# Optimization experiments

Measured on AMD Instinct MI355X. Metric: run time of the kernel, lower is better.

Reference implementation:

```python
import jax, jax.numpy as jnp
import numpy as np

N_NODES = 100000
N_EDGES = 1600000
D = 128


def setup_inputs() -> dict:
    key = jax.random.key(0)
    k1, k2, k3, k4 = jax.random.split(key, 4)
    ego_embeddings = jax.random.normal(k1, (N_NODES, D), dtype=jnp.float32)
    edge_index = jax.random.randint(k2, (2, N_EDGES), 0, N_NODES, dtype=jnp.int64)
    edge_weight = jax.random.uniform(k3, (N_EDGES,), dtype=jnp.float32)
    W = jax.random.normal(k4, (D, D), dtype=jnp.float32) * (1.0 / np.sqrt(D))
    b = jnp.zeros((D,), dtype=jnp.float32)
    return {"ego_embeddings": ego_embeddings, "edge_index": edge_index,
            "edge_weight": edge_weight, "W": W, "b": b}


def reference(ego_embeddings, edge_index, edge_weight, W, b):
    # SpMM: side[i] = sum_j A[i,j] * ego[j], A given as COO (dst=row, src=col)
    src = edge_index[1]
    dst = edge_index[0]
    messages = ego_embeddings[src] * edge_weight[:, None]  # [E, D]
    side_embeddings = jax.ops.segment_sum(messages, dst, num_segments=N_NODES)
    # gcn aggregator: LeakyReLU(Linear(ego + side)); dropout p=0.0 -> identity
    h = (ego_embeddings + side_embeddings) @ W.T + b
    return jax.nn.leaky_relu(h, negative_slope=0.01)
```

## Files before the change

kernel.cpp:

```cpp
#include <hip/hip_runtime.h>

#define N_NODES 100000
#define N_EDGES 1600000
#define DIM 128
#define CAP 48

#define NBIN 1563
#define BINW 64
#define BCAP 1280
#define EPB  8192
#define NBBLK ((N_EDGES + EPB - 1) / EPB)

#define WB_OFF   0
#define GCUR_OFF 32768
#define STG_OFF  65536
#define EGOB_OFF (STG_OFF + (size_t)NBIN * BCAP * 8)
#define WS_BF16  (EGOB_OFF + (size_t)N_NODES * DIM * 2)

#define DEG_OFF  65536
#define EPK_OFF  465536

using short8  = __attribute__((ext_vector_type(8))) short;
using floatx4 = __attribute__((ext_vector_type(4))) float;

static __device__ __forceinline__ unsigned short f2bf(float f) {
    unsigned u = __float_as_uint(f);
    u += 0x7FFF + ((u >> 16) & 1);
    return (unsigned short)(u >> 16);
}
static __device__ __forceinline__ float bf_lo(unsigned u) {
    return __uint_as_float(u << 16);
}
static __device__ __forceinline__ float bf_hi(unsigned u) {
    return __uint_as_float(u & 0xFFFF0000u);
}

#define EGO_BLKS 6250
#define TAIL_BLKS 64
__global__ __launch_bounds__(256) void convert_all(
        const float4* __restrict__ e4, uint4* __restrict__ o4,
        const float* __restrict__ W, unsigned short* __restrict__ Wb,
        int* __restrict__ gcur) {
    const int b = blockIdx.x;
    const int tid = threadIdx.x;
    if (b < EGO_BLKS) {
        int i = b * 256 + tid;
        float4 a = e4[2 * i];
        float4 c = e4[2 * i + 1];
        uint4 o;
        o.x = (unsigned)f2bf(a.x) | ((unsigned)f2bf(a.y) << 16);
        o.y = (unsigned)f2bf(a.z) | ((unsigned)f2bf(a.w) << 16);
        o.z = (unsigned)f2bf(c.x) | ((unsigned)f2bf(c.y) << 16);
        o.w = (unsigned)f2bf(c.z) | ((unsigned)f2bf(c.w) << 16);
        o4[i] = o;
    } else {
        int j = (b - EGO_BLKS) * 256 + tid;
        if (j < DIM * DIM) Wb[j] = f2bf(W[j]);
        if (j < NBIN) gcur[j] = 0;
    }
}

__global__ __launch_bounds__(256) void convert_w(const float* __restrict__ W,
                                                 unsigned short* __restrict__ Wb) {
    int i = blockIdx.x * 256 + threadIdx.x;
    if (i < DIM * DIM) Wb[i] = f2bf(W[i]);
}

__global__ __launch_bounds__(256) void bin2scan(
        const int* __restrict__ eidx,
        const float* __restrict__ ew,
        int* __restrict__ gcur,
        uint2* __restrict__ stg) {
    __shared__ int lh[NBIN];
    __shared__ int gb[NBIN];
    const int tid = threadIdx.x;
    const int b0 = blockIdx.x * EPB;

    for (int i = tid; i < NBIN; i += 256) lh[i] = 0;
    __syncthreads();

    for (int k = 0; k < EPB / 256; ++k) {
        int e = b0 + k * 256 + tid;
        if (e < N_EDGES) atomicAdd(&lh[eidx[e] >> 6], 1);
    }
    __syncthreads();

    for (int i = tid; i < NBIN; i += 256) {
        int c = lh[i];
        gb[i] = c ? atomicAdd(&gcur[i], c) : 0;
        lh[i] = 0;
    }
    __syncthreads();

    for (int k = 0; k < EPB / 256; ++k) {
        int e = b0 + k * 256 + tid;
        if (e < N_EDGES) {
            int d = eidx[e];
            int s = eidx[N_EDGES + e];
            float w = ew[e];
            unsigned rec = ((unsigned)s << 15) | (unsigned)(w * 32767.0f + 0.5f);
            int bin = d >> 6;
            int pos = gb[bin] + atomicAdd(&lh[bin], 1);
            if (pos < BCAP)
                stg[(size_t)bin * BCAP + pos] = make_uint2(rec, (unsigned)d);
        }
    }
}

#define LSTR 136
__global__ __launch_bounds__(256, 5) void bin_gather_gemm(
        const unsigned* __restrict__ eg2,
        const uint2* __restrict__ stg,
        const int* __restrict__ gcur,
        const unsigned short* __restrict__ Wb,
        const float* __restrict__ bias,
        float* __restrict__ out) {
    __shared__ __align__(16) unsigned short s_x[BINW * LSTR];
    __shared__ unsigned s_epk[BINW * CAP];
    __shared__ int s_lc[BINW];

    const int tid  = threadIdx.x;
    const int wave = tid >> 6;
    const int lane = tid & 63;
    const int bin  = blockIdx.x;
    const int R    = bin * BINW;
    const float inv15 = 1.0f / 32767.0f;
    const uint2* eg8 = (const uint2*)eg2;

    if (tid < BINW) s_lc[tid] = 0;
    __syncthreads();

    int cnt = gcur[bin];
    if (cnt > BCAP) cnt = BCAP;
    const uint2* bstg = stg + (size_t)bin * BCAP;
    for (int r = tid; r < cnt; r += 256) {
        uint2 rc = bstg[r];
        int d6 = (int)(rc.y & (BINW - 1));
        int rk = atomicAdd(&s_lc[d6], 1);
        if (rk < CAP) s_epk[d6 * CAP + rk] = rc.x;
    }
    __syncthreads();

    {
        const int half = lane >> 5;
        const int hl   = lane & 31;
        const int plane = (lane < CAP) ? lane : (CAP - 1);

        int lA = wave * 16;
        unsigned pvA = s_epk[lA * CAP + plane];
        unsigned pvB = s_epk[(lA + 1) * CAP + plane];
        int dgA = s_lc[lA];
        int dgB = s_lc[lA + 1];

        for (int i = 0; i < 8; ++i) {
            const int myNode = R + wave * 16 + 2 * i + half;
            const bool valid = myNode < N_NODES;

            unsigned pvAc = pvA, pvBc = pvB;
            int dgAc = dgA < CAP ? dgA : CAP;
            int dgBc = dgB < CAP ? dgB : CAP;
            const int dgme = half ? dgBc : dgAc;
            const int dgw  = dgAc > dgBc ? dgAc : dgBc;

            if (i < 7) {
                int mA = wave * 16 + 2 * (i + 1);
                pvA = s_epk[mA * CAP + plane];
                pvB = s_epk[(mA + 1) * CAP + plane];
                dgA = s_lc[mA];
                dgB = s_lc[mA + 1];
            }

            uint2 idv = make_uint2(0u, 0u);
            if (valid) idv = eg8[(size_t)myNode * 32 + hl];

            float acc[4][4];
#pragma unroll
            for (int k = 0; k < 4; ++k)
#pragma unroll
                for (int c = 0; c < 4; ++c) acc[k][c] = 0.f;
            acc[0][0] = bf_lo(idv.x);  acc[0][1] = bf_hi(idv.x);
            acc[0][2] = bf_lo(idv.y);  acc[0][3] = bf_hi(idv.y);

            for (int e = 0; e < dgw; e += 8) {
                unsigned p[8];
                uint2 g[8];
#pragma unroll
                for (int k = 0; k < 8; ++k) {
                    unsigned pa = __shfl(pvAc, e + k);
                    unsigned pb = __shfl(pvBc, e + k);
                    unsigned ps = half ? pb : pa;
                    p[k] = ((e + k) < dgme) ? ps : 0u;
                }
#pragma unroll
                for (int k = 0; k < 8; ++k)
                    g[k] = eg8[(size_t)(p[k] >> 15) * 32 + hl];
#pragma unroll
                for (int k = 0; k < 8; ++k) {
                    float wv = (float)(p[k] & 0x7FFF) * inv15;
                    acc[k & 3][0] = fmaf(wv, bf_lo(g[k].x), acc[k & 3][0]);
                    acc[k & 3][1] = fmaf(wv, bf_hi(g[k].x), acc[k & 3][1]);
                    acc[k & 3][2] = fmaf(wv, bf_lo(g[k].y), acc[k & 3][2]);
                    acc[k & 3][3] = fmaf(wv, bf_hi(g[k].y), acc[k & 3][3]);
                }
            }

            float s0 = (acc[0][0] + acc[1][0]) + (acc[2][0] + acc[3][0]);
            float s1 = (acc[0][1] + acc[1][1]) + (acc[2][1] + acc[3][1]);
            float s2 = (acc[0][2] + acc[1][2]) + (acc[2][2] + acc[3][2]);
            float s3 = (acc[0][3] + acc[1][3]) + (acc[2][3] + acc[3][3]);

            unsigned lo = (unsigned)f2bf(s0) | ((unsigned)f2bf(s1) << 16);
            unsigned hi = (unsigned)f2bf(s2) | ((unsigned)f2bf(s3) << 16);
            int myRow = wave * 16 + 2 * i + half;
            *(uint2*)&s_x[myRow * LSTR + hl * 4] = make_uint2(lo, hi);
        }
    }

    const int m0 = wave * 16;
    const int ml = lane & 15;
    const int q  = lane >> 4;

    floatx4 acc[8];
#pragma unroll
    for (int nt = 0; nt < 8; ++nt) acc[nt] = (floatx4){0.f, 0.f, 0.f, 0.f};

#pragma unroll
    for (int kc = 0; kc < 4; ++kc) {
        short8 a = *(const short8*)&s_x[(m0 + ml) * LSTR + kc * 32 + q * 8];
#pragma unroll
        for (int nt = 0; nt < 8; ++nt) {
            short8 b = *(const short8*)&Wb[(size_t)(nt * 16 + ml) * DIM + kc * 32 + q * 8];
            acc[nt] = __builtin_amdgcn_mfma_f32_16x16x32_bf16(a, b, acc[nt], 0, 0, 0);
        }
    }

#pragma unroll
    for (int nt = 0; nt < 8; ++nt) {
        int col = nt * 16 + ml;
        float bv = bias[col];
#pragma unroll
        for (int r = 0; r < 4; ++r) {
            int row = R + m0 + q * 4 + r;
            if (row < N_NODES) {
                float v = acc[nt][r] + bv;
                v = v > 0.f ? v : 0.01f * v;
                out[(size_t)row * DIM + col] = v;
            }
        }
    }
}

__global__ __launch_bounds__(256) void csr_scatter(
        const int* __restrict__ eidx,
        const float* __restrict__ ew,
        int* __restrict__ deg,
        unsigned* __restrict__ epk) {
    int e = blockIdx.x * 256 + threadIdx.x;
    if (e >= N_EDGES) return;
    int dst = eidx[e];
    int src = eidx[N_EDGES + e];
    float w = ew[e];
    int r = atomicAdd(&deg[dst], 1);
    if (r < CAP) {
        unsigned q = (unsigned)(w * 32767.0f + 0.5f);
        epk[(size_t)dst * CAP + r] = ((unsigned)src << 15) | q;
    }
}

__global__ __launch_bounds__(256) void gather_gemm_f32(
        const float* __restrict__ egof,
        const unsigned* __restrict__ epk,
        const int* __restrict__ deg,
        const unsigned short* __restrict__ Wb,
        const float* __restrict__ bias,
        float* __restrict__ out) {
    __shared__ __align__(16) unsigned short s_x[64 * LSTR];

    const int tid  = threadIdx.x;
    const int wave = tid >> 6;
    const int lane = tid & 63;
    const int R    = blockIdx.x * 64;
    const float inv15 = 1.0f / 32767.0f;

    for (int i = 0; i < 16; ++i) {
        int node = R + wave * 16 + i;
        float ax = 0.f, ay = 0.f, bx = 0.f, by = 0.f;
        float cx = 0.f, cy = 0.f, dx2 = 0.f, dy2 = 0.f;
        if (node < N_NODES) {
            size_t cidx = (size_t)node * 64 + lane;
            float2 vv = ((const float2*)egof)[cidx];
            ax = vv.x; ay = vv.y;
            int dg = deg[node];
            if (dg > CAP) dg = CAP;
            size_t base = (size_t)node * CAP;
            unsigned pv = epk[base + (lane < CAP ? lane : CAP - 1)];
            int e = 0;
            for (; e + 3 < dg; e += 4) {
                unsigned p0 = __shfl(pv, e + 0);
                unsigned p1 = __shfl(pv, e + 1);
                unsigned p2 = __shfl(pv, e + 2);
                unsigned p3 = __shfl(pv, e + 3);
                float2 v0 = ((const float2*)egof)[(size_t)(p0 >> 15) * 64 + lane];
                float2 v1 = ((const float2*)egof)[(size_t)(p1 >> 15) * 64 + lane];
                float2 v2 = ((const float2*)egof)[(size_t)(p2 >> 15) * 64 + lane];
                float2 v3 = ((const float2*)egof)[(size_t)(p3 >> 15) * 64 + lane];
                float w0 = (float)(p0 & 0x7FFF) * inv15;
                float w1 = (float)(p1 & 0x7FFF) * inv15;
                float w2 = (float)(p2 & 0x7FFF) * inv15;
                float w3 = (float)(p3 & 0x7FFF) * inv15;
                ax = fmaf(w0, v0.x, ax);  ay = fmaf(w0, v0.y, ay);
                bx = fmaf(w1, v1.x, bx);  by = fmaf(w1, v1.y, by);
                cx = fmaf(w2, v2.x, cx);  cy = fmaf(w2, v2.y, cy);
                dx2 = fmaf(w3, v3.x, dx2); dy2 = fmaf(w3, v3.y, dy2);
            }
            for (; e < dg; ++e) {
                unsigned p = __shfl(pv, e);
                float2 vv2 = ((const float2*)egof)[(size_t)(p >> 15) * 64 + lane];
                float w = (float)(p & 0x7FFF) * inv15;
                ax = fmaf(w, vv2.x, ax);  ay = fmaf(w, vv2.y, ay);
            }
        }
        unsigned pk = (unsigned)f2bf(ax + bx + cx + dx2) |
                      ((unsigned)f2bf(ay + by + cy + dy2) << 16);
        *(unsigned*)&s_x[(wave * 16 + i) * LSTR + 2 * lane] = pk;
    }

    const int m0 = wave * 16;
    const int ml = lane & 15;
    const int q  = lane >> 4;

    floatx4 acc[8];
#pragma unroll
    for (int nt = 0; nt < 8; ++nt) acc[nt] = (floatx4){0.f, 0.f, 0.f, 0.f};

#pragma unroll
    for (int kc = 0; kc < 4; ++kc) {
        short8 a = *(const short8*)&s_x[(m0 + ml) * LSTR + kc * 32 + q * 8];
#pragma unroll
        for (int nt = 0; nt < 8; ++nt) {
            short8 b = *(const short8*)&Wb[(size_t)(nt * 16 + ml) * DIM + kc * 32 + q * 8];
            acc[nt] = __builtin_amdgcn_mfma_f32_16x16x32_bf16(a, b, acc[nt], 0, 0, 0);
        }
    }

#pragma unroll
    for (int nt = 0; nt < 8; ++nt) {
        int col = nt * 16 + ml;
        float bv = bias[col];
#pragma unroll
        for (int r = 0; r < 4; ++r) {
            int row = R + m0 + q * 4 + r;
            if (row < N_NODES) {
                float v = acc[nt][r] + bv;
                v = v > 0.f ? v : 0.01f * v;
                out[(size_t)row * DIM + col] = v;
            }
        }
    }
}

extern "C" void kernel_launch(void* const* d_in, const int* in_sizes, int n_in,
                              void* d_out, int out_size, void* d_ws, size_t ws_size,
                              hipStream_t stream) {
    const float* ego  = (const float*)d_in[0];
    const int*   eidx = (const int*)d_in[1];
    const float* ew   = (const float*)d_in[2];
    const float* W    = (const float*)d_in[3];
    const float* bias = (const float*)d_in[4];
    float* out = (float*)d_out;

    char* ws = (char*)d_ws;
    unsigned short* Wb   = (unsigned short*)(ws + WB_OFF);
    int*            gcur = (int*)(ws + GCUR_OFF);
    uint2*          stg  = (uint2*)(ws + STG_OFF);
    unsigned short* egob = (unsigned short*)(ws + EGOB_OFF);

    const bool use_bf16 = (ws_size >= WS_BF16);

    if (use_bf16) {
        convert_all<<<EGO_BLKS + TAIL_BLKS, 256, 0, stream>>>(
            (const float4*)ego, (uint4*)egob, W, Wb, gcur);
        bin2scan<<<NBBLK, 256, 0, stream>>>(eidx, ew, gcur, stg);
        bin_gather_gemm<<<NBIN, 256, 0, stream>>>(
            (const unsigned*)egob, stg, gcur, Wb, bias, out);
    } else {
        int*      deg = (int*)(ws + DEG_OFF);
        unsigned* epk = (unsigned*)(ws + EPK_OFF);
        convert_w<<<(DIM * DIM + 255) / 256, 256, 0, stream>>>(W, Wb);
        hipMemsetAsync(deg, 0, (size_t)N_NODES * sizeof(int), stream);
        csr_scatter<<<(N_EDGES + 255) / 256, 256, 0, stream>>>(
            eidx, ew, deg, epk);
        gather_gemm_f32<<<(N_NODES + 63) / 64, 256, 0, stream>>>(
            ego, epk, deg, Wb, bias, out);
    }
}
```

Baseline: 270.9 us.

## Use coarse 512-row edge bins and XCD-aware bin mapping in gather kernel

```diff
diff --git a/kernel.cpp b/kernel.cpp
--- a/kernel.cpp
+++ b/kernel.cpp
@@ -7,14 +7,16 @@
 
 #define NBIN 1563
 #define BINW 64
-#define BCAP 1280
+#define NBIN_C 196
+#define CBW 512
+#define BCAP_C 8960
 #define EPB  8192
 #define NBBLK ((N_EDGES + EPB - 1) / EPB)
 
 #define WB_OFF   0
 #define GCUR_OFF 32768
 #define STG_OFF  65536
-#define EGOB_OFF (STG_OFF + (size_t)NBIN * BCAP * 8)
+#define EGOB_OFF (STG_OFF + (size_t)NBIN_C * BCAP_C * 8)
 #define WS_BF16  (EGOB_OFF + (size_t)N_NODES * DIM * 2)
 
 #define DEG_OFF  65536
@@ -56,7 +58,7 @@
     } else {
         int j = (b - EGO_BLKS) * 256 + tid;
         if (j < DIM * DIM) Wb[j] = f2bf(W[j]);
-        if (j < NBIN) gcur[j] = 0;
+        if (j < NBIN_C * 16) gcur[j] = 0;
     }
 }
 
@@ -66,29 +68,29 @@
     if (i < DIM * DIM) Wb[i] = f2bf(W[i]);
 }
 
-__global__ __launch_bounds__(256) void bin2scan(
+__global__ __launch_bounds__(256) void coarse_bin(
         const int* __restrict__ eidx,
         const float* __restrict__ ew,
         int* __restrict__ gcur,
         uint2* __restrict__ stg) {
-    __shared__ int lh[NBIN];
-    __shared__ int gb[NBIN];
+    __shared__ int lh[NBIN_C];
+    __shared__ int gb[NBIN_C];
     const int tid = threadIdx.x;
     const int b0 = blockIdx.x * EPB;
 
-    for (int i = tid; i < NBIN; i += 256) lh[i] = 0;
+    if (tid < NBIN_C) lh[tid] = 0;
     __syncthreads();
 
     for (int k = 0; k < EPB / 256; ++k) {
         int e = b0 + k * 256 + tid;
-        if (e < N_EDGES) atomicAdd(&lh[eidx[e] >> 6], 1);
+        if (e < N_EDGES) atomicAdd(&lh[eidx[e] >> 9], 1);
     }
     __syncthreads();
 
-    for (int i = tid; i < NBIN; i += 256) {
-        int c = lh[i];
-        gb[i] = c ? atomicAdd(&gcur[i], c) : 0;
-        lh[i] = 0;
+    if (tid < NBIN_C) {
+        int c = lh[tid];
+        gb[tid] = c ? atomicAdd(&gcur[tid * 16], c) : 0;
+        lh[tid] = 0;
     }
     __syncthreads();
 
@@ -99,10 +101,10 @@
             int s = eidx[N_EDGES + e];
             float w = ew[e];
             unsigned rec = ((unsigned)s << 15) | (unsigned)(w * 32767.0f + 0.5f);
-            int bin = d >> 6;
+            int bin = d >> 9;
             int pos = gb[bin] + atomicAdd(&lh[bin], 1);
-            if (pos < BCAP)
-                stg[(size_t)bin * BCAP + pos] = make_uint2(rec, (unsigned)d);
+            if (pos < BCAP_C)
+                stg[(size_t)bin * BCAP_C + pos] = make_uint2(rec, (unsigned)d);
         }
     }
 }
@@ -122,22 +124,31 @@
     const int tid  = threadIdx.x;
     const int wave = tid >> 6;
     const int lane = tid & 63;
-    const int bin  = blockIdx.x;
+
+    const int bid = blockIdx.x;
+    const int xq = NBIN / 8, xr = NBIN % 8;
+    const int xcd = bid & 7, xi = bid >> 3;
+    const int bin = (xcd < xr ? xcd * (xq + 1)
+                              : xr * (xq + 1) + (xcd - xr) * xq) + xi;
+
     const int R    = bin * BINW;
+    const int cbin = bin >> 3;
     const float inv15 = 1.0f / 32767.0f;
     const uint2* eg8 = (const uint2*)eg2;
 
     if (tid < BINW) s_lc[tid] = 0;
     __syncthreads();
 
-    int cnt = gcur[bin];
-    if (cnt > BCAP) cnt = BCAP;
-    const uint2* bstg = stg + (size_t)bin * BCAP;
-    for (int r = tid; r < cnt; r += 256) {
-        uint2 rc = bstg[r];
-        int d6 = (int)(rc.y & (BINW - 1));
-        int rk = atomicAdd(&s_lc[d6], 1);
-        if (rk < CAP) s_epk[d6 * CAP + rk] = rc.x;
+    int ccnt = gcur[cbin * 16];
+    if (ccnt > BCAP_C) ccnt = BCAP_C;
+    const uint2* cwin = stg + (size_t)cbin * BCAP_C;
+    for (int r = tid; r < ccnt; r += 256) {
+        uint2 rc = cwin[r];
+        if ((int)(rc.y >> 6) == bin) {
+            int d6 = (int)(rc.y & (BINW - 1));
+            int rk = atomicAdd(&s_lc[d6], 1);
+            if (rk < CAP) s_epk[d6 * CAP + rk] = rc.x;
+        }
     }
     __syncthreads();
 
@@ -380,7 +391,7 @@
     if (use_bf16) {
         convert_all<<<EGO_BLKS + TAIL_BLKS, 256, 0, stream>>>(
             (const float4*)ego, (uint4*)egob, W, Wb, gcur);
-        bin2scan<<<NBBLK, 256, 0, stream>>>(eidx, ew, gcur, stg);
+        coarse_bin<<<NBBLK, 256, 0, stream>>>(eidx, ew, gcur, stg);
         bin_gather_gemm<<<NBIN, 256, 0, stream>>>(
             (const unsigned*)egob, stg, gcur, Wb, bias, out);
     } else {
```

New measurement: 268.9 us. Within noise of the previous version (-0.8%).

## Fuse bf16 conversion and edge binning into one pre-pass kernel with padded counters

Applied to the files above, without the earlier changes.

```diff
diff --git a/kernel.cpp b/kernel.cpp
--- a/kernel.cpp
+++ b/kernel.cpp
@@ -8,17 +8,19 @@
 #define NBIN 1563
 #define BINW 64
 #define BCAP 1280
-#define EPB  8192
-#define NBBLK ((N_EDGES + EPB - 1) / EPB)
+#define EPT  8
+#define EPB  2048
+#define BIN_BLKS ((N_EDGES + EPB - 1) / EPB)
 
 #define WB_OFF   0
 #define GCUR_OFF 32768
-#define STG_OFF  65536
+#define GCUR_BYTES (NBIN * 64)
+#define STG_OFF  139264
 #define EGOB_OFF (STG_OFF + (size_t)NBIN * BCAP * 8)
 #define WS_BF16  (EGOB_OFF + (size_t)N_NODES * DIM * 2)
 
-#define DEG_OFF  65536
-#define EPK_OFF  465536
+#define DEG_OFF  165536
+#define EPK_OFF  565536
 
 using short8  = __attribute__((ext_vector_type(8))) short;
 using floatx4 = __attribute__((ext_vector_type(4))) float;
@@ -36,13 +38,20 @@
 }
 
 #define EGO_BLKS 6250
-#define TAIL_BLKS 64
-__global__ __launch_bounds__(256) void convert_all(
+#define W_BLKS   64
+#define PRE_BLKS (EGO_BLKS + W_BLKS + BIN_BLKS)
+__global__ __launch_bounds__(256) void fused_pre(
         const float4* __restrict__ e4, uint4* __restrict__ o4,
         const float* __restrict__ W, unsigned short* __restrict__ Wb,
-        int* __restrict__ gcur) {
+        const int* __restrict__ eidx,
+        const float* __restrict__ ew,
+        int* __restrict__ gcur,
+        uint2* __restrict__ stg) {
+    __shared__ int lh[NBIN];
+    __shared__ int gb[NBIN];
     const int b = blockIdx.x;
     const int tid = threadIdx.x;
+
     if (b < EGO_BLKS) {
         int i = b * 256 + tid;
         float4 a = e4[2 * i];
@@ -53,10 +62,50 @@
         o.z = (unsigned)f2bf(c.x) | ((unsigned)f2bf(c.y) << 16);
         o.w = (unsigned)f2bf(c.z) | ((unsigned)f2bf(c.w) << 16);
         o4[i] = o;
-    } else {
+        return;
+    }
+    if (b < EGO_BLKS + W_BLKS) {
         int j = (b - EGO_BLKS) * 256 + tid;
         if (j < DIM * DIM) Wb[j] = f2bf(W[j]);
-        if (j < NBIN) gcur[j] = 0;
+        return;
+    }
+
+    const int b0 = (b - EGO_BLKS - W_BLKS) * EPB;
+
+    for (int i = tid; i < NBIN; i += 256) lh[i] = 0;
+    __syncthreads();
+
+    int dst[EPT], rank[EPT];
+    unsigned rec[EPT];
+    bool val[EPT];
+#pragma unroll
+    for (int k = 0; k < EPT; ++k) {
+        int e = b0 + k * 256 + tid;
+        val[k] = e < N_EDGES;
+        int ec = val[k] ? e : 0;
+        int d = eidx[ec];
+        int s = eidx[N_EDGES + ec];
+        float w = ew[ec];
+        dst[k] = d;
+        rec[k] = ((unsigned)s << 15) | (unsigned)(w * 32767.0f + 0.5f);
+        rank[k] = val[k] ? atomicAdd(&lh[d >> 6], 1) : 0;
+    }
+    __syncthreads();
+
+    for (int i = tid; i < NBIN; i += 256) {
+        int c = lh[i];
+        gb[i] = c ? atomicAdd(&gcur[i * 16], c) : 0;
+    }
+    __syncthreads();
+
+#pragma unroll
+    for (int k = 0; k < EPT; ++k) {
+        if (val[k]) {
+            int bin = dst[k] >> 6;
+            int pos = gb[bin] + rank[k];
+            if (pos < BCAP)
+                stg[(size_t)bin * BCAP + pos] = make_uint2(rec[k], (unsigned)dst[k]);
+        }
     }
 }
 
@@ -64,47 +113,6 @@
                                                  unsigned short* __restrict__ Wb) {
     int i = blockIdx.x * 256 + threadIdx.x;
     if (i < DIM * DIM) Wb[i] = f2bf(W[i]);
-}
-
-__global__ __launch_bounds__(256) void bin2scan(
-        const int* __restrict__ eidx,
-        const float* __restrict__ ew,
-        int* __restrict__ gcur,
-        uint2* __restrict__ stg) {
-    __shared__ int lh[NBIN];
-    __shared__ int gb[NBIN];
-    const int tid = threadIdx.x;
-    const int b0 = blockIdx.x * EPB;
-
-    for (int i = tid; i < NBIN; i += 256) lh[i] = 0;
-    __syncthreads();
-
-    for (int k = 0; k < EPB / 256; ++k) {
-        int e = b0 + k * 256 + tid;
-        if (e < N_EDGES) atomicAdd(&lh[eidx[e] >> 6], 1);
-    }
-    __syncthreads();
-
-    for (int i = tid; i < NBIN; i += 256) {
-        int c = lh[i];
-        gb[i] = c ? atomicAdd(&gcur[i], c) : 0;
-        lh[i] = 0;
-    }
-    __syncthreads();
-
-    for (int k = 0; k < EPB / 256; ++k) {
-        int e = b0 + k * 256 + tid;
-        if (e < N_EDGES) {
-            int d = eidx[e];
-            int s = eidx[N_EDGES + e];
-            float w = ew[e];
-            unsigned rec = ((unsigned)s << 15) | (unsigned)(w * 32767.0f + 0.5f);
-            int bin = d >> 6;
-            int pos = gb[bin] + atomicAdd(&lh[bin], 1);
-            if (pos < BCAP)
-                stg[(size_t)bin * BCAP + pos] = make_uint2(rec, (unsigned)d);
-        }
-    }
 }
 
 #define LSTR 136
@@ -130,7 +138,7 @@
     if (tid < BINW) s_lc[tid] = 0;
     __syncthreads();
 
-    int cnt = gcur[bin];
+    int cnt = gcur[bin * 16];
     if (cnt > BCAP) cnt = BCAP;
     const uint2* bstg = stg + (size_t)bin * BCAP;
     for (int r = tid; r < cnt; r += 256) {
@@ -378,9 +386,9 @@
     const bool use_bf16 = (ws_size >= WS_BF16);
 
     if (use_bf16) {
-        convert_all<<<EGO_BLKS + TAIL_BLKS, 256, 0, stream>>>(
-            (const float4*)ego, (uint4*)egob, W, Wb, gcur);
-        bin2scan<<<NBBLK, 256, 0, stream>>>(eidx, ew, gcur, stg);
+        hipMemsetAsync(gcur, 0, GCUR_BYTES, stream);
+        fused_pre<<<PRE_BLKS, 256, 0, stream>>>(
+            (const float4*)ego, (uint4*)egob, W, Wb, eidx, ew, gcur, stg);
         bin_gather_gemm<<<NBIN, 256, 0, stream>>>(
             (const unsigned*)egob, stg, gcur, Wb, bias, out);
     } else {
```

Measured after the change: 267.8 us. No clear change (-1.2%).

## Fuse binning and conversion into one pre-kernel with padded bin counters

Applied to the files above, without the earlier changes.

```diff
diff --git a/kernel.cpp b/kernel.cpp
--- a/kernel.cpp
+++ b/kernel.cpp
@@ -8,17 +8,18 @@
 #define NBIN 1563
 #define BINW 64
 #define BCAP 1280
-#define EPB  8192
-#define NBBLK ((N_EDGES + EPB - 1) / EPB)
+#define EPB  12512
+#define BIN_BLKS 128
 
 #define WB_OFF   0
 #define GCUR_OFF 32768
-#define STG_OFF  65536
+#define GCUR_BYTES (NBIN * 64)
+#define STG_OFF  139264
 #define EGOB_OFF (STG_OFF + (size_t)NBIN * BCAP * 8)
 #define WS_BF16  (EGOB_OFF + (size_t)N_NODES * DIM * 2)
 
-#define DEG_OFF  65536
-#define EPK_OFF  465536
+#define DEG_OFF  165536
+#define EPK_OFF  565536
 
 using short8  = __attribute__((ext_vector_type(8))) short;
 using floatx4 = __attribute__((ext_vector_type(4))) float;
@@ -36,64 +37,66 @@
 }
 
 #define EGO_BLKS 6250
-#define TAIL_BLKS 64
-__global__ __launch_bounds__(256) void convert_all(
+#define W_BLKS   64
+#define PRE_BLKS (BIN_BLKS + EGO_BLKS + W_BLKS)
+__global__ __launch_bounds__(256) void fused_pre(
         const float4* __restrict__ e4, uint4* __restrict__ o4,
         const float* __restrict__ W, unsigned short* __restrict__ Wb,
-        int* __restrict__ gcur) {
-    const int b = blockIdx.x;
-    const int tid = threadIdx.x;
-    if (b < EGO_BLKS) {
-        int i = b * 256 + tid;
-        float4 a = e4[2 * i];
-        float4 c = e4[2 * i + 1];
-        uint4 o;
-        o.x = (unsigned)f2bf(a.x) | ((unsigned)f2bf(a.y) << 16);
-        o.y = (unsigned)f2bf(a.z) | ((unsigned)f2bf(a.w) << 16);
-        o.z = (unsigned)f2bf(c.x) | ((unsigned)f2bf(c.y) << 16);
-        o.w = (unsigned)f2bf(c.z) | ((unsigned)f2bf(c.w) << 16);
-        o4[i] = o;
-    } else {
-        int j = (b - EGO_BLKS) * 256 + tid;
-        if (j < DIM * DIM) Wb[j] = f2bf(W[j]);
-        if (j < NBIN) gcur[j] = 0;
-    }
-}
-
-__global__ __launch_bounds__(256) void convert_w(const float* __restrict__ W,
-                                                 unsigned short* __restrict__ Wb) {
-    int i = blockIdx.x * 256 + threadIdx.x;
-    if (i < DIM * DIM) Wb[i] = f2bf(W[i]);
-}
-
-__global__ __launch_bounds__(256) void bin2scan(
         const int* __restrict__ eidx,
         const float* __restrict__ ew,
         int* __restrict__ gcur,
         uint2* __restrict__ stg) {
     __shared__ int lh[NBIN];
     __shared__ int gb[NBIN];
+    const int b = blockIdx.x;
     const int tid = threadIdx.x;
-    const int b0 = blockIdx.x * EPB;
+
+    if (b >= BIN_BLKS) {
+        const int cb = b - BIN_BLKS;
+        if (cb < EGO_BLKS) {
+            int i = cb * 256 + tid;
+            float4 a = e4[2 * i];
+            float4 c = e4[2 * i + 1];
+            uint4 o;
+            o.x = (unsigned)f2bf(a.x) | ((unsigned)f2bf(a.y) << 16);
+            o.y = (unsigned)f2bf(a.z) | ((unsigned)f2bf(a.w) << 16);
+            o.z = (unsigned)f2bf(c.x) | ((unsigned)f2bf(c.y) << 16);
+            o.w = (unsigned)f2bf(c.z) | ((unsigned)f2bf(c.w) << 16);
+            o4[i] = o;
+        } else {
+            int j = (cb - EGO_BLKS) * 256 + tid;
+            if (j < DIM * DIM) Wb[j] = f2bf(W[j]);
+        }
+        return;
+    }
+
+    const int b0 = b * EPB;
 
     for (int i = tid; i < NBIN; i += 256) lh[i] = 0;
     __syncthreads();
 
-    for (int k = 0; k < EPB / 256; ++k) {
-        int e = b0 + k * 256 + tid;
-        if (e < N_EDGES) atomicAdd(&lh[eidx[e] >> 6], 1);
+    for (int base = b0 + tid * 4; base < b0 + EPB; base += 1024) {
+        if (base + 3 < N_EDGES) {
+            int4 d4 = *(const int4*)&eidx[base];
+            atomicAdd(&lh[d4.x >> 6], 1);
+            atomicAdd(&lh[d4.y >> 6], 1);
+            atomicAdd(&lh[d4.z >> 6], 1);
+            atomicAdd(&lh[d4.w >> 6], 1);
+        } else {
+            for (int j = 0; j < 4; ++j)
+                if (base + j < N_EDGES) atomicAdd(&lh[eidx[base + j] >> 6], 1);
+        }
     }
     __syncthreads();
 
     for (int i = tid; i < NBIN; i += 256) {
         int c = lh[i];
-        gb[i] = c ? atomicAdd(&gcur[i], c) : 0;
+        gb[i] = c ? atomicAdd(&gcur[i * 16], c) : 0;
         lh[i] = 0;
     }
     __syncthreads();
 
-    for (int k = 0; k < EPB / 256; ++k) {
-        int e = b0 + k * 256 + tid;
+    for (int e = b0 + tid; e < b0 + EPB; e += 256) {
         if (e < N_EDGES) {
             int d = eidx[e];
             int s = eidx[N_EDGES + e];
@@ -105,6 +108,12 @@
                 stg[(size_t)bin * BCAP + pos] = make_uint2(rec, (unsigned)d);
         }
     }
+}
+
+__global__ __launch_bounds__(256) void convert_w(const float* __restrict__ W,
+                                                 unsigned short* __restrict__ Wb) {
+    int i = blockIdx.x * 256 + threadIdx.x;
+    if (i < DIM * DIM) Wb[i] = f2bf(W[i]);
 }
 
 #define LSTR 136
@@ -130,7 +139,7 @@
     if (tid < BINW) s_lc[tid] = 0;
     __syncthreads();
 
-    int cnt = gcur[bin];
+    int cnt = gcur[bin * 16];
     if (cnt > BCAP) cnt = BCAP;
     const uint2* bstg = stg + (size_t)bin * BCAP;
     for (int r = tid; r < cnt; r += 256) {
@@ -378,9 +387,9 @@
     const bool use_bf16 = (ws_size >= WS_BF16);
 
     if (use_bf16) {
-        convert_all<<<EGO_BLKS + TAIL_BLKS, 256, 0, stream>>>(
-            (const float4*)ego, (uint4*)egob, W, Wb, gcur);
-        bin2scan<<<NBBLK, 256, 0, stream>>>(eidx, ew, gcur, stg);
+        hipMemsetAsync(gcur, 0, GCUR_BYTES, stream);
+        fused_pre<<<PRE_BLKS, 256, 0, stream>>>(
+            (const float4*)ego, (uint4*)egob, W, Wb, eidx, ew, gcur, stg);
         bin_gather_gemm<<<NBIN, 256, 0, stream>>>(
             (const unsigned*)egob, stg, gcur, Wb, bias, out);
     } else {
```

Result: no change. 274.2 us (+1.2%).
